# Optimization experiments

Measured on AMD Instinct MI355X. Metric: run time of the kernel, lower is better.

## Reference

```python
import jax, jax.numpy as jnp
import numpy as np

B, S, D, H = 4, 2048, 1024, 16
DK = D // H
SCALE = float(np.sqrt(DK))
NEG_INF = jnp.float32(-1e30)


def setup_inputs() -> dict:
    key = jax.random.key(0)
    ks = jax.random.split(key, 12)
    std = 1.0 / np.sqrt(D)
    def lin(k):
        kw, kb = jax.random.split(k)
        W = jax.random.uniform(kw, (D, D), jnp.float32, -std, std)
        b = jax.random.uniform(kb, (D,), jnp.float32, -std, std)
        return W, b
    Wq, bq = lin(ks[0]); Wk, bk = lin(ks[1]); Wv, bv = lin(ks[2]); Wo, bo = lin(ks[3])
    query = jax.random.normal(ks[4], (B, S, D), jnp.float32)
    key_t = jax.random.normal(ks[5], (B, S, D), jnp.float32)
    value = jax.random.normal(ks[6], (B, S, D), jnp.float32)
    # causal mask, broadcastable to [B,H,S,S]; positions where mask==0 are blocked
    mask = jnp.tril(jnp.ones((S, S), dtype=bool))[None, None]
    return {"query": query, "key": key_t, "value": value,
            "Wq": Wq, "bq": bq, "Wk": Wk, "bk": bk, "Wv": Wv, "bv": bv,
            "Wo": Wo, "bo": bo, "mask": mask}


def reference(query, key, value, Wq, bq, Wk, bk, Wv, bv, Wo, bo, mask):
    # projections: x @ W.T + b (torch nn.Linear convention)
    q = (query @ Wq.T + bq).reshape(B, S, H, DK).transpose(0, 2, 1, 3)  # [B,H,S,DK]
    k = (key @ Wk.T + bk).reshape(B, S, H, DK).transpose(0, 2, 1, 3)
    v = (value @ Wv.T + bv).reshape(B, S, H, DK).transpose(0, 2, 1, 3)
    scores = jnp.einsum('bhqd,bhkd->bhqk', q, k) / SCALE  # [B,H,S,S]
    scores = jnp.where(mask, scores, NEG_INF)
    attn = jax.nn.softmax(scores, axis=-1)
    # dropout is identity in eval / p used at train only; omitted (p treated as 0)
    context = jnp.einsum('bhqk,bhkd->bhqd', attn, v)  # [B,H,S,DK]
    context = context.transpose(0, 2, 1, 3).reshape(B, S, D)
    return context @ Wo.T + bo
```

## Files before the change

kernel.cpp:

```cpp
#include <hip/hip_runtime.h>
#include <hip/hip_bf16.h>
#include <cstdint>
#include <cstddef>


namespace {

constexpr int B  = 4;
constexpr int S  = 2048;
constexpr int D  = 1024;
constexpr int H  = 16;
constexpr int DK = 64;
constexpr int M  = B * S;
constexpr float LOG2E     = 1.44269504088896f;
constexpr float QSCALE    = 0.125f * LOG2E;
constexpr float NEG_BIG   = -1e30f;
constexpr float DEFER_THR = 8.0f;

using bf16 = __hip_bfloat16;

typedef __attribute__((ext_vector_type(8))) __bf16 bf16x8;
typedef __attribute__((ext_vector_type(4))) float  f32x4;

__device__ __forceinline__ uint16_t f2bfu(float x) {
  uint32_t a = __builtin_bit_cast(uint32_t, x);
  return (uint16_t)((a + 0x7FFFu + ((a >> 16) & 1u)) >> 16);
}
__device__ __forceinline__ uint32_t pk2(float x, float y) {
  return (uint32_t)f2bfu(x) | ((uint32_t)f2bfu(y) << 16);
}
__device__ __forceinline__ float ex2(float x) {
  float r; asm("v_exp_f32 %0, %1" : "=v"(r) : "v"(x)); return r;
}
__device__ __forceinline__ uint32_t cvtpk(float lo, float hi) {
  uint32_t r;
  asm("v_cvt_pk_bf16_f32 %0, %1, %2" : "=v"(r) : "v"(lo), "v"(hi));
  return r;
}
__device__ __forceinline__ float hmax4(f32x4 v) {
  return fmaxf(fmaxf(v[0], v[1]), fmaxf(v[2], v[3]));
}

__device__ __forceinline__ void ldst16(const uint4* g, uint4* l) {
  __builtin_amdgcn_global_load_lds(
      (const __attribute__((address_space(1))) void*)g,
      (__attribute__((address_space(3))) void*)l, 16, 0, 0);
}

__global__ __launch_bounds__(256)
void cvt3(const float* __restrict__ a, const float* __restrict__ b,
          const float* __restrict__ c, bf16* __restrict__ x,
          bf16* __restrict__ y, bf16* __restrict__ z_, int n8)
{
  const int zz = blockIdx.y;
  const float* src = (zz == 0) ? a : (zz == 1) ? b : c;
  bf16*        dst = (zz == 0) ? x : (zz == 1) ? y : z_;
  const int i = blockIdx.x * 256 + threadIdx.x;
  if (i >= n8) return;
  const float4 p = ((const float4*)src)[2 * i];
  const float4 q = ((const float4*)src)[2 * i + 1];
  uint4 r;
  r.x = pk2(p.x, p.y); r.y = pk2(p.z, p.w);
  r.z = pk2(q.x, q.y); r.w = pk2(q.z, q.w);
  ((uint4*)dst)[i] = r;
}

template <int MODE>
__global__ __launch_bounds__(256)
void gemm128(const bf16* __restrict__ A, const bf16* __restrict__ Wb,
             const float* __restrict__ bias, void* __restrict__ out,
             int N, int K, float scale)
{
  __shared__ uint4 AsU[2][1024];
  __shared__ uint4 BsU[2][1024];

  const int tid  = threadIdx.x;
  const int w    = tid >> 6;
  const int lane = tid & 63;
  const int lm   = lane & 15;
  const int quad = lane >> 4;
  const int wm   = (w >> 1) * 64;
  const int wn   = (w & 1) * 64;

  const int row0 = blockIdx.y * 128, col0 = blockIdx.x * 128;
  const int g8 = K >> 3;

  const uint4* Ag = (const uint4*)A + (size_t)row0 * g8;
  const uint4* Bg = (const uint4*)Wb + (size_t)col0 * g8;

  f32x4 acc[4][4] = {};
  const int KT = K / 64;

#pragma unroll
  for (int i = 0; i < 4; ++i) {
    const int chunk = i * 256 + w * 64 + lane;
    const int r = chunk >> 3, c = chunk & 7;
    ldst16(&Ag[(size_t)r * g8 + c], &AsU[0][i * 256 + w * 64]);
    ldst16(&Bg[(size_t)r * g8 + c], &BsU[0][i * 256 + w * 64]);
  }

  int cur = 0;
  for (int kt = 0; kt < KT; ++kt) {
    __syncthreads();
    if (kt + 1 < KT) {
#pragma unroll
      for (int i = 0; i < 4; ++i) {
        const int chunk = i * 256 + w * 64 + lane;
        const int r = chunk >> 3, c = chunk & 7;
        ldst16(&Ag[(size_t)r * g8 + (kt + 1) * 8 + c], &AsU[cur ^ 1][i * 256 + w * 64]);
        ldst16(&Bg[(size_t)r * g8 + (kt + 1) * 8 + c], &BsU[cur ^ 1][i * 256 + w * 64]);
      }
    }
#pragma unroll
    for (int kk = 0; kk < 2; ++kk) {
      bf16x8 af[4], bfr[4];
#pragma unroll
      for (int tm = 0; tm < 4; ++tm)
        af[tm] = __builtin_bit_cast(bf16x8, AsU[cur][(wm + tm * 16 + lm) * 8 + kk * 4 + quad]);
#pragma unroll
      for (int tn = 0; tn < 4; ++tn)
        bfr[tn] = __builtin_bit_cast(bf16x8, BsU[cur][(wn + tn * 16 + lm) * 8 + kk * 4 + quad]);
#pragma unroll
      for (int tm = 0; tm < 4; ++tm)
#pragma unroll
        for (int tn = 0; tn < 4; ++tn)
          acc[tm][tn] = __builtin_amdgcn_mfma_f32_16x16x32_bf16(af[tm], bfr[tn], acc[tm][tn], 0, 0, 0);
    }
    cur ^= 1;
  }

#pragma unroll
  for (int tm = 0; tm < 4; ++tm) {
#pragma unroll
    for (int tn = 0; tn < 4; ++tn) {
      const int col = col0 + wn + tn * 16 + lm;
      const float bv = bias[col];
      if (MODE == 2) {
        float vv[4];
#pragma unroll
        for (int r = 0; r < 4; ++r) vv[r] = (acc[tm][tn][r] + bv) * scale;
        const int s0 = row0 + wm + tm * 16 + quad * 4;
        const int b_ = s0 >> 11, ss = s0 & (S - 1);
        const int h_ = col >> 6, dk = col & (DK - 1);
        uint2 st; st.x = pk2(vv[0], vv[1]); st.y = pk2(vv[2], vv[3]);
        *(uint2*)((bf16*)out + (((size_t)b_ * H + h_) * DK + dk) * S + ss) = st;
      } else {
#pragma unroll
        for (int r = 0; r < 4; ++r) {
          const int row = row0 + wm + tm * 16 + quad * 4 + r;
          const float v = (acc[tm][tn][r] + bv) * scale;
          if (MODE == 0) {
            ((float*)out)[(size_t)row * N + col] = v;
          } else {
            const int b_ = row >> 11, s_ = row & (S - 1);
            const int h_ = col >> 6,  dk = col & (DK - 1);
            ((bf16*)out)[(((size_t)b_ * H + h_) * S + s_) * DK + dk] =
                __builtin_bit_cast(bf16, f2bfu(v));
          }
        }
      }
    }
  }
}

__global__ __launch_bounds__(512)
void flash_mfma(const bf16* __restrict__ Q, const bf16* __restrict__ K,
                const bf16* __restrict__ Vt, bf16* __restrict__ ctx)
{
  __shared__ uint4 KsU[2][512];
  __shared__ uint4 VtU[2][512];
  __shared__ uint16_t Os[128 * 72];

  const int tid  = threadIdx.x;
  const int w    = tid >> 6;
  const int lane = tid & 63;
  const int lm   = lane & 15;
  const int quad = lane >> 4;
  const int bh   = blockIdx.x;
  const int pr   = blockIdx.y;
  const size_t base = (size_t)bh * S * DK;

  const uint4* Kg0 = (const uint4*)(K + base);
  const uint4* Vg0 = (const uint4*)(Vt + (size_t)bh * DK * S);

  const int rr  = w * 8 + (lane >> 3);
  const int csw = (lane & 7) ^ (lane >> 3) ^ ((w & 1) << 2);
  const int fv  = (lm & 7) ^ (((lm >> 3) & 1) << 2);
  const int r0  = ((lm >> 2) << 3) | (lm & 3);

  uint16_t* const Ow = Os + (w * 16) * 72;
  const int b_ = bh >> 4, h_ = bh & (H - 1);

  for (int pass = 0; pass < 2; ++pass) {
    const int qi = pass ? (15 - pr) : pr;
    const int q0 = qi * 128;
    const int qbase = q0 + w * 16;

    bf16x8 qf0, qf1;
    {
      const bf16* qrow = Q + base + (size_t)(qbase + lm) * DK;
      qf0 = __builtin_bit_cast(bf16x8, *(const uint4*)(qrow + quad * 8));
      qf1 = __builtin_bit_cast(bf16x8, *(const uint4*)(qrow + 32 + quad * 8));
    }

    f32x4 o[4] = {};
    float m_i = NEG_BIG, l_i = 0.f;

    const int nt = 2 * qi + 2;

    ldst16(&Kg0[(size_t)rr * 8 + csw],       &KsU[0][w * 64]);
    ldst16(&Vg0[(size_t)rr * (S / 8) + csw], &VtU[0][w * 64]);

    int cur = 0;
    for (int t = 0; t < nt; ++t) {
      __syncthreads();
      if (t + 1 < nt) {
        const int k1 = (t + 1) * 64;
        ldst16(&Kg0[(size_t)(k1 + rr) * 8 + csw],         &KsU[cur ^ 1][w * 64]);
        ldst16(&Vg0[(size_t)rr * (S / 8) + k1 / 8 + csw], &VtU[cur ^ 1][w * 64]);
      }
      const int k0 = t * 64;
      if (k0 <= qbase + 15) {
        const uint4* Ks = KsU[cur];
        const uint4* Vs = VtU[cur];

        f32x4 sc[4];
        __builtin_amdgcn_s_setprio(1);
#pragma unroll
        for (int tn = 0; tn < 4; ++tn) {
          const int row = r0 + ((tn & 1) << 2) + ((tn >> 1) << 5);
          const int fr  = (row & 7) ^ (((row >> 3) & 1) << 2);
          const int cb  = quad ^ fr;
          bf16x8 kb0 = __builtin_bit_cast(bf16x8, Ks[row * 8 + cb]);
          bf16x8 kb1 = __builtin_bit_cast(bf16x8, Ks[row * 8 + (cb ^ 4)]);
          sc[tn] = __builtin_amdgcn_mfma_f32_16x16x32_bf16(
                       kb0, qf0, f32x4{0.f, 0.f, 0.f, 0.f}, 0, 0, 0);
          sc[tn] = __builtin_amdgcn_mfma_f32_16x16x32_bf16(kb1, qf1, sc[tn], 0, 0, 0);
        }
        __builtin_amdgcn_s_setprio(0);

        if (k0 + 63 > qbase) {
          const int qg = qbase + lm;
#pragma unroll
          for (int tn = 0; tn < 4; ++tn) {
            const int kb_ = k0 + ((tn >> 1) << 5) + (quad << 3) + ((tn & 1) << 2);
#pragma unroll
            for (int r = 0; r < 4; ++r)
              if (kb_ + r > qg) sc[tn][r] = NEG_BIG;
          }
        }

        float mloc = fmaxf(fmaxf(hmax4(sc[0]), hmax4(sc[1])),
                           fmaxf(hmax4(sc[2]), hmax4(sc[3])));
        mloc = fmaxf(mloc, __shfl_xor(mloc, 16));
        mloc = fmaxf(mloc, __shfl_xor(mloc, 32));

        if (__any(mloc > m_i + DEFER_THR)) {
          const float mn = fmaxf(m_i, mloc);
          const float al = ex2(m_i - mn);
          l_i *= al; m_i = mn;
          const float a0 = __shfl(al, quad * 4 + 0, 16);
          const float a1 = __shfl(al, quad * 4 + 1, 16);
          const float a2 = __shfl(al, quad * 4 + 2, 16);
          const float a3 = __shfl(al, quad * 4 + 3, 16);
#pragma unroll
          for (int tn = 0; tn < 4; ++tn) {
            o[tn][0] *= a0; o[tn][1] *= a1; o[tn][2] *= a2; o[tn][3] *= a3;
          }
        }

        float ls = 0.f;
#pragma unroll
        for (int tn = 0; tn < 4; ++tn) {
#pragma unroll
          for (int r = 0; r < 4; ++r) sc[tn][r] = ex2(sc[tn][r] - m_i);
          ls += (sc[tn][0] + sc[tn][1]) + (sc[tn][2] + sc[tn][3]);
        }
        l_i += ls;

        uint4 pw0, pw1;
        pw0.x = cvtpk(sc[0][0], sc[0][1]); pw0.y = cvtpk(sc[0][2], sc[0][3]);
        pw0.z = cvtpk(sc[1][0], sc[1][1]); pw0.w = cvtpk(sc[1][2], sc[1][3]);
        pw1.x = cvtpk(sc[2][0], sc[2][1]); pw1.y = cvtpk(sc[2][2], sc[2][3]);
        pw1.z = cvtpk(sc[3][0], sc[3][1]); pw1.w = cvtpk(sc[3][2], sc[3][3]);
        const bf16x8 ap0 = __builtin_bit_cast(bf16x8, pw0);
        const bf16x8 ap1 = __builtin_bit_cast(bf16x8, pw1);

        __builtin_amdgcn_s_setprio(1);
#pragma unroll
        for (int tn = 0; tn < 4; ++tn) {
          const int vrow = tn * 16 + lm;
          const int cv = quad ^ fv;
          bf16x8 vb0 = __builtin_bit_cast(bf16x8, Vs[vrow * 8 + cv]);
          bf16x8 vb1 = __builtin_bit_cast(bf16x8, Vs[vrow * 8 + (cv ^ 4)]);
          o[tn] = __builtin_amdgcn_mfma_f32_16x16x32_bf16(ap0, vb0, o[tn], 0, 0, 0);
          o[tn] = __builtin_amdgcn_mfma_f32_16x16x32_bf16(ap1, vb1, o[tn], 0, 0, 0);
        }
        __builtin_amdgcn_s_setprio(0);
      }
      cur ^= 1;
    }

    __syncthreads();
    {
      float lr = l_i;
      lr += __shfl_xor(lr, 16);
      lr += __shfl_xor(lr, 32);
      const float inv = 1.f / lr;
      const float i0 = __shfl(inv, quad * 4 + 0, 16);
      const float i1 = __shfl(inv, quad * 4 + 1, 16);
      const float i2 = __shfl(inv, quad * 4 + 2, 16);
      const float i3 = __shfl(inv, quad * 4 + 3, 16);
#pragma unroll
      for (int tn = 0; tn < 4; ++tn) {
        Ow[(quad * 4 + 0) * 72 + tn * 16 + lm] = f2bfu(o[tn][0] * i0);
        Ow[(quad * 4 + 1) * 72 + tn * 16 + lm] = f2bfu(o[tn][1] * i1);
        Ow[(quad * 4 + 2) * 72 + tn * 16 + lm] = f2bfu(o[tn][2] * i2);
        Ow[(quad * 4 + 3) * 72 + tn * 16 + lm] = f2bfu(o[tn][3] * i3);
      }
    }
    __syncthreads();

#pragma unroll
    for (int i = 0; i < 2; ++i) {
      const int idx = tid + i * 512;
      const int row = idx >> 3, c = idx & 7;
      const uint4 v = *(const uint4*)(Os + row * 72 + c * 8);
      *(uint4*)(ctx + ((((size_t)b_ * S + q0 + row) * H + h_) << 6) + c * 8) = v;
    }
  }
}

}

extern "C" void kernel_launch(void* const* d_in, const int* in_sizes, int n_in,
                              void* d_out, int out_size, void* d_ws, size_t ws_size,
                              hipStream_t stream)
{
  const float* query = (const float*)d_in[0];
  const float* key_  = (const float*)d_in[1];
  const float* value = (const float*)d_in[2];
  const float* Wq    = (const float*)d_in[3];
  const float* bq    = (const float*)d_in[4];
  const float* Wk    = (const float*)d_in[5];
  const float* bk    = (const float*)d_in[6];
  const float* Wv    = (const float*)d_in[7];
  const float* bv    = (const float*)d_in[8];
  const float* Wo    = (const float*)d_in[9];
  const float* bo    = (const float*)d_in[10];

  const size_t qkv = (size_t)B * H * S * DK;
  const size_t DD  = (size_t)D * D;
  bf16* slot0 = (bf16*)d_ws;
  bf16* slot1 = slot0 + qkv;
  bf16* slot2 = slot1 + qkv;
  bf16* slot3 = slot2 + qkv;
  bf16* dout0 = (bf16*)d_out;
  bf16* dout1 = dout0 + qkv;

  const int n8in = (int)(qkv / 8);
  const int n8w  = (int)(DD / 8);
  const dim3 gproj(D / 128, M / 128);
  const dim3 gattn(B * H, 8);

  cvt3<<<dim3(n8in / 256, 3), 256, 0, stream>>>(query, key_, value,
                                                dout0, dout1, slot3, n8in);
  cvt3<<<dim3(n8w / 256, 2), 256, 0, stream>>>(Wq, Wk, Wk,
                                               slot2, slot2 + DD, slot2, n8w);
  gemm128<1><<<gproj, 256, 0, stream>>>(dout0, slot2, bq, slot0, D, D, QSCALE);
  gemm128<1><<<gproj, 256, 0, stream>>>(dout1, slot2 + DD, bk, slot1, D, D, 1.0f);
  cvt3<<<dim3(n8w / 256, 1), 256, 0, stream>>>(Wv, Wv, Wv,
                                               dout0, dout0, dout0, n8w);
  gemm128<2><<<gproj, 256, 0, stream>>>(slot3, dout0, bv, slot2, D, D, 1.0f);
  flash_mfma<<<gattn, 512, 0, stream>>>(slot0, slot1, slot2, slot3);
  cvt3<<<dim3(n8w / 256, 1), 256, 0, stream>>>(Wo, Wo, Wo,
                                               slot0, slot0, slot0, n8w);
  gemm128<0><<<gproj, 256, 0, stream>>>(slot3, slot0, bo, d_out, D, D, 1.0f);
}
```

Before: 343.4 us.

## Batch weight conversion and fuse Q/K/V projections into one launch

Converts all four weight matrices to bf16 in a single launch and runs the three Q/K/V projection GEMMs as one grid with a z dimension selecting the input, weights, bias and output layout. This cuts kernel launches and gives a single larger grid with more blocks in flight, helping tail utilisation. The new GEMM is single-buffered in shared memory (the old one had two LDS buffers) and uses launch_bounds(256,3). The path depends on the workspace being large enough, otherwise the old sequence runs.

After: 325.8 us. 1.05x faster.

```diff
diff --git a/kernel.cpp b/kernel.cpp
--- a/kernel.cpp
+++ b/kernel.cpp
@@ -65,6 +65,114 @@
   ((uint4*)dst)[i] = r;
 }
 
+__global__ __launch_bounds__(256)
+void cvt4(const float* __restrict__ a, const float* __restrict__ b,
+          const float* __restrict__ c, const float* __restrict__ d,
+          bf16* __restrict__ dst, int n8)
+{
+  const int zz = blockIdx.y;
+  const float* src = (zz == 0) ? a : (zz == 1) ? b : (zz == 2) ? c : d;
+  bf16* out = dst + (size_t)zz * n8 * 8;
+  const int i = blockIdx.x * 256 + threadIdx.x;
+  if (i >= n8) return;
+  const float4 p = ((const float4*)src)[2 * i];
+  const float4 q = ((const float4*)src)[2 * i + 1];
+  uint4 r;
+  r.x = pk2(p.x, p.y); r.y = pk2(p.z, p.w);
+  r.z = pk2(q.x, q.y); r.w = pk2(q.z, q.w);
+  ((uint4*)out)[i] = r;
+}
+
+__global__ __launch_bounds__(256, 3)
+void proj_qkv(const bf16* __restrict__ Aq, const bf16* __restrict__ Ak,
+              const bf16* __restrict__ Av, const bf16* __restrict__ Wall,
+              const float* __restrict__ bq_, const float* __restrict__ bk_,
+              const float* __restrict__ bv_, bf16* __restrict__ qo,
+              bf16* __restrict__ ko, bf16* __restrict__ vto)
+{
+  __shared__ uint4 AsU[1024];
+  __shared__ uint4 BsU[1024];
+
+  const int z = blockIdx.z;
+  const bf16*  A    = (z == 0) ? Aq : (z == 1) ? Ak : Av;
+  const bf16*  Wb   = Wall + (size_t)z * D * D;
+  const float* bias = (z == 0) ? bq_ : (z == 1) ? bk_ : bv_;
+
+  const int tid  = threadIdx.x;
+  const int w    = tid >> 6;
+  const int lane = tid & 63;
+  const int lm   = lane & 15;
+  const int quad = lane >> 4;
+  const int wm   = (w >> 1) * 64;
+  const int wn   = (w & 1) * 64;
+
+  const int row0 = blockIdx.y * 128, col0 = blockIdx.x * 128;
+  constexpr int g8 = D >> 3;
+
+  const uint4* Ag = (const uint4*)A + (size_t)row0 * g8;
+  const uint4* Bg = (const uint4*)Wb + (size_t)col0 * g8;
+
+  f32x4 acc[4][4] = {};
+
+  for (int kt = 0; kt < D / 64; ++kt) {
+    __syncthreads();
+#pragma unroll
+    for (int i = 0; i < 4; ++i) {
+      const int chunk = i * 256 + w * 64 + lane;
+      const int r = chunk >> 3, c = chunk & 7;
+      ldst16(&Ag[(size_t)r * g8 + kt * 8 + c], &AsU[i * 256 + w * 64]);
+      ldst16(&Bg[(size_t)r * g8 + kt * 8 + c], &BsU[i * 256 + w * 64]);
+    }
+    __syncthreads();
+#pragma unroll
+    for (int kk = 0; kk < 2; ++kk) {
+      bf16x8 af[4], bfr[4];
+#pragma unroll
+      for (int tm = 0; tm < 4; ++tm)
+        af[tm] = __builtin_bit_cast(bf16x8, AsU[(wm + tm * 16 + lm) * 8 + kk * 4 + quad]);
+#pragma unroll
+      for (int tn = 0; tn < 4; ++tn)
+        bfr[tn] = __builtin_bit_cast(bf16x8, BsU[(wn + tn * 16 + lm) * 8 + kk * 4 + quad]);
+#pragma unroll
+      for (int tm = 0; tm < 4; ++tm)
+#pragma unroll
+        for (int tn = 0; tn < 4; ++tn)
+          acc[tm][tn] = __builtin_amdgcn_mfma_f32_16x16x32_bf16(af[tm], bfr[tn], acc[tm][tn], 0, 0, 0);
+    }
+  }
+
+  const float scale = (z == 0) ? QSCALE : 1.0f;
+#pragma unroll
+  for (int tm = 0; tm < 4; ++tm) {
+#pragma unroll
+    for (int tn = 0; tn < 4; ++tn) {
+      const int col = col0 + wn + tn * 16 + lm;
+      const float bv = bias[col];
+      if (z == 2) {
+        float vv[4];
+#pragma unroll
+        for (int r = 0; r < 4; ++r) vv[r] = acc[tm][tn][r] + bv;
+        const int s0 = row0 + wm + tm * 16 + quad * 4;
+        const int b_ = s0 >> 11, ss = s0 & (S - 1);
+        const int h_ = col >> 6, dk = col & (DK - 1);
+        uint2 st; st.x = pk2(vv[0], vv[1]); st.y = pk2(vv[2], vv[3]);
+        *(uint2*)(vto + (((size_t)b_ * H + h_) * DK + dk) * S + ss) = st;
+      } else {
+        bf16* out = (z == 0) ? qo : ko;
+#pragma unroll
+        for (int r = 0; r < 4; ++r) {
+          const int row = row0 + wm + tm * 16 + quad * 4 + r;
+          const float v = (acc[tm][tn][r] + bv) * scale;
+          const int b_ = row >> 11, s_ = row & (S - 1);
+          const int h_ = col >> 6,  dk = col & (DK - 1);
+          out[(((size_t)b_ * H + h_) * S + s_) * DK + dk] =
+              __builtin_bit_cast(bf16, f2bfu(v));
+        }
+      }
+    }
+  }
+}
+
 template <int MODE>
 __global__ __launch_bounds__(256)
 void gemm128(const bf16* __restrict__ A, const bf16* __restrict__ Wb,
@@ -355,6 +463,7 @@
   bf16* slot1 = slot0 + qkv;
   bf16* slot2 = slot1 + qkv;
   bf16* slot3 = slot2 + qkv;
+  bf16* slot4 = slot3 + qkv;
   bf16* dout0 = (bf16*)d_out;
   bf16* dout1 = dout0 + qkv;
 
@@ -363,17 +472,30 @@
   const dim3 gproj(D / 128, M / 128);
   const dim3 gattn(B * H, 8);
 
-  cvt3<<<dim3(n8in / 256, 3), 256, 0, stream>>>(query, key_, value,
-                                                dout0, dout1, slot3, n8in);
-  cvt3<<<dim3(n8w / 256, 2), 256, 0, stream>>>(Wq, Wk, Wk,
-                                               slot2, slot2 + DD, slot2, n8w);
-  gemm128<1><<<gproj, 256, 0, stream>>>(dout0, slot2, bq, slot0, D, D, QSCALE);
-  gemm128<1><<<gproj, 256, 0, stream>>>(dout1, slot2 + DD, bk, slot1, D, D, 1.0f);
-  cvt3<<<dim3(n8w / 256, 1), 256, 0, stream>>>(Wv, Wv, Wv,
-                                               dout0, dout0, dout0, n8w);
-  gemm128<2><<<gproj, 256, 0, stream>>>(slot3, dout0, bv, slot2, D, D, 1.0f);
-  flash_mfma<<<gattn, 512, 0, stream>>>(slot0, slot1, slot2, slot3);
-  cvt3<<<dim3(n8w / 256, 1), 256, 0, stream>>>(Wo, Wo, Wo,
-                                               slot0, slot0, slot0, n8w);
-  gemm128<0><<<gproj, 256, 0, stream>>>(slot3, slot0, bo, d_out, D, D, 1.0f);
-}
+  const size_t need = (4 * qkv + 4 * DD) * sizeof(bf16);
+
+  if (ws_size >= need) {
+    cvt3<<<dim3(n8in / 256, 3), 256, 0, stream>>>(query, key_, value,
+                                                  dout0, dout1, slot3, n8in);
+    cvt4<<<dim3(n8w / 256, 4), 256, 0, stream>>>(Wq, Wk, Wv, Wo, slot4, n8w);
+    proj_qkv<<<dim3(D / 128, M / 128, 3), 256, 0, stream>>>(
+        dout0, dout1, slot3, slot4, bq, bk, bv, slot0, slot1, slot2);
+    flash_mfma<<<gattn, 512, 0, stream>>>(slot0, slot1, slot2, slot3);
+    gemm128<0><<<gproj, 256, 0, stream>>>(slot3, slot4 + 3 * DD, bo, d_out,
+                                          D, D, 1.0f);
+  } else {
+    cvt3<<<dim3(n8in / 256, 3), 256, 0, stream>>>(query, key_, value,
+                                                  dout0, dout1, slot3, n8in);
+    cvt3<<<dim3(n8w / 256, 2), 256, 0, stream>>>(Wq, Wk, Wk,
+                                                 slot2, slot2 + DD, slot2, n8w);
+    gemm128<1><<<gproj, 256, 0, stream>>>(dout0, slot2, bq, slot0, D, D, QSCALE);
+    gemm128<1><<<gproj, 256, 0, stream>>>(dout1, slot2 + DD, bk, slot1, D, D, 1.0f);
+    cvt3<<<dim3(n8w / 256, 1), 256, 0, stream>>>(Wv, Wv, Wv,
+                                                 dout0, dout0, dout0, n8w);
+    gemm128<2><<<gproj, 256, 0, stream>>>(slot3, dout0, bv, slot2, D, D, 1.0f);
+    flash_mfma<<<gattn, 512, 0, stream>>>(slot0, slot1, slot2, slot3);
+    cvt3<<<dim3(n8w / 256, 1), 256, 0, stream>>>(Wo, Wo, Wo,
+                                                 slot0, slot0, slot0, n8w);
+    gemm128<0><<<gproj, 256, 0, stream>>>(slot3, slot0, bo, d_out, D, D, 1.0f);
+  }
+}
```
